# Kernel optimization log

Hardware: AMD Instinct MI355X
Metric: run time of the kernel (lower is better)

The kernel has to match this reference:

```python
import jax, jax.numpy as jnp
import numpy as np

B, N, E = 4, 10000, 160000
IN, OUT, H, ED = 64, 128, 2, 1
SLOPE = 0.2  # GATv2Conv default negative_slope


def _seg_softmax(logits, seg, n):
    # logits: [Ef, H]; softmax over edges sharing the same dst node, per head
    m = jax.ops.segment_max(logits, seg, num_segments=n)
    e = jnp.exp(logits - m[seg])
    d = jax.ops.segment_sum(e, seg, num_segments=n)
    return e / d[seg]


def setup_inputs() -> dict:
    key = jax.random.key(0)
    ks = jax.random.split(key, 10)
    s = 0.05
    return {
        "node_feats": jax.random.normal(ks[0], (B, N, IN), jnp.float32),
        "edge_index": jax.random.randint(ks[1], (2, E), 0, N, dtype=jnp.int64),
        "edge_attr": jax.random.normal(ks[2], (E, ED), jnp.float32),
        "Wl": jax.random.normal(ks[3], (IN, H * OUT), jnp.float32) * s,
        "bl": jax.random.normal(ks[4], (H * OUT,), jnp.float32) * s,
        "Wr": jax.random.normal(ks[5], (IN, H * OUT), jnp.float32) * s,
        "br": jax.random.normal(ks[6], (H * OUT,), jnp.float32) * s,
        "We": jax.random.normal(ks[7], (ED, H * OUT), jnp.float32) * s,
        "att": jax.random.normal(ks[8], (H, OUT), jnp.float32) * s,
        "bias": jax.random.normal(ks[9], (H * OUT,), jnp.float32) * s,
    }


def reference(node_feats, edge_index, edge_attr, Wl, bl, Wr, br, We, att, bias):
    src, dst = edge_index[0], edge_index[1]
    # PyG add_self_loops(fill_value='mean'): self-loop attr = mean of incoming edge attrs per node
    ones = jnp.ones((E,), edge_attr.dtype)
    deg = jax.ops.segment_sum(ones, dst, num_segments=N)
    loop_attr = jax.ops.segment_sum(edge_attr, dst, num_segments=N) / jnp.maximum(deg, 1.0)[:, None]
    sl = jnp.arange(N)
    src_f = jnp.concatenate([src, sl])           # [Ef] with Ef = E + N
    dst_f = jnp.concatenate([dst, sl])
    e_feat = (jnp.concatenate([edge_attr, loop_attr], axis=0) @ We).reshape(-1, H, OUT)  # [Ef,H,C]

    xl = (node_feats @ Wl + bl).reshape(B, N, H, OUT)  # lin_l(x)
    xr = (node_feats @ Wr + br).reshape(B, N, H, OUT)  # lin_r(x)

    # GATv2: score on leaky_relu(x_l[src] + x_r[dst] + lin_edge(e))
    msg = jax.nn.leaky_relu(xl[:, src_f] + xr[:, dst_f] + e_feat[None], SLOPE)  # [B,Ef,H,C]
    logits = jnp.einsum('behc,hc->beh', msg, att)                               # [B,Ef,H]
    alpha = jax.vmap(lambda l: _seg_softmax(l, dst_f, N))(logits)               # [B,Ef,H]

    weighted = alpha[..., None] * xl[:, src_f]                                  # [B,Ef,H,C]
    out = jax.vmap(lambda w: jax.ops.segment_sum(w, dst_f, num_segments=N))(weighted)  # [B,N,H,C]
    return out.reshape(B, N, H * OUT) + bias
```

## Files before the change

### kernel.cpp

```cpp
#include <hip/hip_runtime.h>
#include <hip/hip_bf16.h>

#define BQ 4
#define NN 10000
#define EE 160000
#define HC 256
#define SLOPEK 0.2f
#define CAPE 128

typedef __attribute__((ext_vector_type(8))) short bf16x8;
typedef __attribute__((ext_vector_type(4))) float f32x4;

__device__ __forceinline__ unsigned short f2bf(float f) {
    unsigned int u = __float_as_uint(f);
    u = (u + 0x7FFFu + ((u >> 16) & 1u)) >> 16;
    return (unsigned short)u;
}
__device__ __forceinline__ float bflo(unsigned int u) { return __uint_as_float(u << 16); }
__device__ __forceinline__ float bfhi(unsigned int u) { return __uint_as_float(u & 0xFFFF0000u); }

__global__ __launch_bounds__(256) void k_wpack(
    const float* __restrict__ Wl, const float* __restrict__ bl,
    const float* __restrict__ Wr, const float* __restrict__ br,
    unsigned short* __restrict__ wp, float* __restrict__ bp)
{
    const int tid = blockIdx.x * 256 + threadIdx.x;
    if (tid < 32768) {
        const int j  = tid & 7;
        const int l  = (tid >> 3) & 63;
        const int s  = (tid >> 9) & 1;
        const int ct = tid >> 10;
        const int col = ct * 16 + (l & 15);
        const int kk  = s * 32 + ((l >> 4) << 3) + j;
        const float w = (col < 256) ? Wl[kk * 256 + col] : Wr[kk * 256 + (col - 256)];
        wp[tid] = f2bf(w);
    } else if (tid < 32768 + 512) {
        const int c = tid - 32768;
        bp[c] = (c < 256) ? bl[c] : br[c - 256];
    }
}

__global__ __launch_bounds__(256) void k_pre(
    const float* __restrict__ x, const unsigned short* __restrict__ wp,
    const float* __restrict__ bp,
    unsigned short* __restrict__ xl, unsigned short* __restrict__ xr,
    const int* __restrict__ ei, const float* __restrict__ ea,
    int* __restrict__ cnt, float* __restrict__ asum,
    int* __restrict__ csrc, float* __restrict__ cattr)
{
    if (blockIdx.x >= 625) {
        const int e = (blockIdx.x - 625) * 256 + threadIdx.x;
        const int   sn = ei[e];
        const int   d  = ei[EE + e];
        const float a  = ea[e];
        const int pos  = atomicAdd(&cnt[d], 1);
        atomicAdd(&asum[d], a);
        if (pos < CAPE - 1) {
            csrc[d * CAPE + pos]  = sn << 10;
            cattr[d * CAPE + pos] = a;
        }
        return;
    }
    const int w = threadIdx.x >> 6, l = threadIdx.x & 63;
    const int row0 = blockIdx.x * 64 + w * 16;
    const int arow = row0 + (l & 15);
    const float* xp = x + (size_t)arow * 64 + ((l >> 4) << 3);

    bf16x8 a[2];
#pragma unroll
    for (int s = 0; s < 2; ++s) {
        const float4 lo = *reinterpret_cast<const float4*>(xp + s * 32);
        const float4 hi = *reinterpret_cast<const float4*>(xp + s * 32 + 4);
        union { bf16x8 v; unsigned short u[8]; } t;
        t.u[0] = f2bf(lo.x); t.u[1] = f2bf(lo.y); t.u[2] = f2bf(lo.z); t.u[3] = f2bf(lo.w);
        t.u[4] = f2bf(hi.x); t.u[5] = f2bf(hi.y); t.u[6] = f2bf(hi.z); t.u[7] = f2bf(hi.w);
        a[s] = t.v;
    }
    const int colb = l & 15;
    const int rsub = (l >> 4) << 2;

    for (int g = 0; g < 8; ++g) {
        f32x4 acc[4] = {{0.f,0.f,0.f,0.f},{0.f,0.f,0.f,0.f},
                        {0.f,0.f,0.f,0.f},{0.f,0.f,0.f,0.f}};
#pragma unroll
        for (int c = 0; c < 4; ++c) {
            const int ct = g * 4 + c;
            const bf16x8 b0 = *reinterpret_cast<const bf16x8*>(wp + (((ct * 2 + 0) * 64 + l) << 3));
            const bf16x8 b1 = *reinterpret_cast<const bf16x8*>(wp + (((ct * 2 + 1) * 64 + l) << 3));
            acc[c] = __builtin_amdgcn_mfma_f32_16x16x32_bf16(a[0], b0, acc[c], 0, 0, 0);
            acc[c] = __builtin_amdgcn_mfma_f32_16x16x32_bf16(a[1], b1, acc[c], 0, 0, 0);
        }
#pragma unroll
        for (int c = 0; c < 4; ++c) {
            const int col = (g * 4 + c) * 16 + colb;
            const float bv = bp[col];
#pragma unroll
            for (int r = 0; r < 4; ++r) {
                const int row = row0 + rsub + r;
                const int bb = (row >= 20000) ? (row >= 30000 ? 3 : 2)
                                              : (row >= 10000 ? 1 : 0);
                const int n = row - bb * NN;
                const unsigned short h = f2bf(acc[c][r] + bv);
                if (col < 256) xl[(((size_t)(n * 4 + bb)) << 8) + col] = h;
                else           xr[(((size_t)(n * 4 + bb)) << 8) + (col - 256)] = h;
            }
        }
    }
}

__global__ __launch_bounds__(256, 4) void k_gat(
    const unsigned short* __restrict__ xl, const unsigned short* __restrict__ xr,
    const int* __restrict__ cnt, const float* __restrict__ asum,
    const int* __restrict__ csrc, const float* __restrict__ cattr,
    const float* __restrict__ We, const float* __restrict__ att,
    const float* __restrict__ bias, float* __restrict__ outp)
{
    const int t  = threadIdx.x;
    const int wv = t >> 6, ln = t & 63;
    const int n  = blockIdx.x * 4 + wv;
    const int c  = ln & 15;
    const int b  = ln >> 4;
    const int ch0 = c << 4;

    int dg = cnt[n];
    if (dg > 63) dg = 63;
    int   ms = csrc[n * CAPE + ln];
    float ma = cattr[n * CAPE + ln];
    if (ln == dg) {
        ms = n << 10;
        ma = asum[n] / fmaxf((float)dg, 1.0f);
    }
    const int ntot = dg + 1;

    float we16[16], at16[16], xr16[16], acc[16];
    {
        const float4* Wp = reinterpret_cast<const float4*>(We + ch0);
        const float4* Ap = reinterpret_cast<const float4*>(att + ch0);
#pragma unroll
        for (int j = 0; j < 4; ++j) {
            const float4 w4 = Wp[j], a4 = Ap[j];
            we16[4*j+0] = w4.x; we16[4*j+1] = w4.y; we16[4*j+2] = w4.z; we16[4*j+3] = w4.w;
            at16[4*j+0] = a4.x; at16[4*j+1] = a4.y; at16[4*j+2] = a4.z; at16[4*j+3] = a4.w;
        }
        const uint4* Xp = reinterpret_cast<const uint4*>(
            xr + ((size_t)n << 10) + (b << 8) + ch0);
        const uint4 r0 = Xp[0], r1 = Xp[1];
        xr16[0]=bflo(r0.x); xr16[1]=bfhi(r0.x); xr16[2]=bflo(r0.y); xr16[3]=bfhi(r0.y);
        xr16[4]=bflo(r0.z); xr16[5]=bfhi(r0.z); xr16[6]=bflo(r0.w); xr16[7]=bfhi(r0.w);
        xr16[8]=bflo(r1.x); xr16[9]=bfhi(r1.x); xr16[10]=bflo(r1.y); xr16[11]=bfhi(r1.y);
        xr16[12]=bflo(r1.z); xr16[13]=bfhi(r1.z); xr16[14]=bflo(r1.w); xr16[15]=bfhi(r1.w);
    }
#pragma unroll
    for (int k = 0; k < 16; ++k) acc[k] = 0.f;
    float sh = 0.f;

    const unsigned short* __restrict__ xlp = xl + (b << 8) + ch0;

    int   s0 = __builtin_amdgcn_readlane(ms, 0);
    float a0 = __int_as_float(__builtin_amdgcn_readlane(__float_as_int(ma), 0));
    const unsigned short* pp = xlp + s0;
    uint4 A  = *reinterpret_cast<const uint4*>(pp);
    uint4 Bv = *reinterpret_cast<const uint4*>(pp + 8);

    for (int i = 0; i < ntot; ++i) {
        const int ip = (i + 1 < ntot) ? i + 1 : i;
        const int   s1 = __builtin_amdgcn_readlane(ms, ip);
        const float a1 = __int_as_float(__builtin_amdgcn_readlane(__float_as_int(ma), ip));
        const unsigned short* pn = xlp + s1;
        const uint4 A2 = *reinterpret_cast<const uint4*>(pn);
        const uint4 B2 = *reinterpret_cast<const uint4*>(pn + 8);

        float xv[16];
        xv[0]=bflo(A.x);  xv[1]=bfhi(A.x);  xv[2]=bflo(A.y);  xv[3]=bfhi(A.y);
        xv[4]=bflo(A.z);  xv[5]=bfhi(A.z);  xv[6]=bflo(A.w);  xv[7]=bfhi(A.w);
        xv[8]=bflo(Bv.x); xv[9]=bfhi(Bv.x); xv[10]=bflo(Bv.y); xv[11]=bfhi(Bv.y);
        xv[12]=bflo(Bv.z); xv[13]=bfhi(Bv.z); xv[14]=bflo(Bv.w); xv[15]=bfhi(Bv.w);

        float q[4];
#pragma unroll
        for (int g = 0; g < 4; ++g) {
            float v = fmaf(a0, we16[4*g], xv[4*g] + xr16[4*g]);
            v = fmaf(SLOPEK - 1.f, fminf(v, 0.f), v);
            float qq = v * at16[4*g];
#pragma unroll
            for (int k = 1; k < 4; ++k) {
                float u = fmaf(a0, we16[4*g+k], xv[4*g+k] + xr16[4*g+k]);
                u = fmaf(SLOPEK - 1.f, fminf(u, 0.f), u);
                qq = fmaf(u, at16[4*g+k], qq);
            }
            q[g] = qq;
        }
        float p = (q[0] + q[1]) + (q[2] + q[3]);
        p += __shfl_xor(p, 1);
        p += __shfl_xor(p, 2);
        p += __shfl_xor(p, 4);
        const float e = __expf(p);
        sh += e;
#pragma unroll
        for (int k = 0; k < 16; ++k) acc[k] = fmaf(e, xv[k], acc[k]);

        A = A2; Bv = B2; a0 = a1;
    }

    const float inv = 1.0f / sh;
    float* ob = outp + (((size_t)(b * NN + n)) << 8) + ch0;
    const float4* Bp = reinterpret_cast<const float4*>(bias + ch0);
#pragma unroll
    for (int j = 0; j < 4; ++j) {
        const float4 b4 = Bp[j];
        float4 o;
        o.x = fmaf(acc[4*j+0], inv, b4.x);
        o.y = fmaf(acc[4*j+1], inv, b4.y);
        o.z = fmaf(acc[4*j+2], inv, b4.z);
        o.w = fmaf(acc[4*j+3], inv, b4.w);
        reinterpret_cast<float4*>(ob)[j] = o;
    }
}

extern "C" void kernel_launch(void* const* d_in, const int* in_sizes, int n_in,
                              void* d_out, int out_size, void* d_ws, size_t ws_size,
                              hipStream_t stream)
{
    (void)in_sizes; (void)n_in; (void)out_size; (void)ws_size;
    const float* x    = (const float*)d_in[0];
    const int*   ei   = (const int*)d_in[1];
    const float* ea   = (const float*)d_in[2];
    const float* Wl   = (const float*)d_in[3];
    const float* bl   = (const float*)d_in[4];
    const float* Wr   = (const float*)d_in[5];
    const float* br   = (const float*)d_in[6];
    const float* We   = (const float*)d_in[7];
    const float* att  = (const float*)d_in[8];
    const float* bias = (const float*)d_in[9];
    float* outp = (float*)d_out;

    const size_t R = (size_t)BQ * NN;
    unsigned short* xl16 = (unsigned short*)d_ws;
    unsigned short* xr16 = xl16 + R * HC;
    int*   cnt   = (int*)(xr16 + R * HC);
    float* asum  = (float*)(cnt + NN);
    int*   csrc  = (int*)(asum + NN);
    float* cattr = (float*)(csrc + (size_t)NN * CAPE);
    unsigned short* wp = (unsigned short*)(cattr + (size_t)NN * CAPE);
    float* bp    = (float*)(wp + 32768);

    hipMemsetAsync(cnt, 0, sizeof(int) * NN * 2, stream);

    k_wpack<<<130, 256, 0, stream>>>(Wl, bl, Wr, br, wp, bp);
    k_pre  <<<1250, 256, 0, stream>>>(x, wp, bp, xl16, xr16,
                                      ei, ea, cnt, asum, csrc, cattr);
    k_gat  <<<NN / 4, 256, 0, stream>>>(xl16, xr16, cnt, asum, csrc, cattr,
                                        We, att, bias, outp);
}
```

Baseline: 99.56 us.

## Split each node's edge loop across four wavefronts and pack edge metadata

The GAT kernel now assigns one destination node per block, and its four wavefronts each process every fourth incoming edge. Partial softmax numerators and denominators are then combined through shared memory before the output is written. Edge source offset and attribute are packed into a single int2 array, so each edge needs one store and one load instead of two. The split shortens the serial per-node edge chain and quadruples the grid, at the cost of a block barrier, shared-memory traffic, and four times the redundant setup loads of xr, We and att per node.

```diff
diff --git a/kernel.cpp b/kernel.cpp
--- a/kernel.cpp
+++ b/kernel.cpp
@@ -46,7 +46,7 @@
     unsigned short* __restrict__ xl, unsigned short* __restrict__ xr,
     const int* __restrict__ ei, const float* __restrict__ ea,
     int* __restrict__ cnt, float* __restrict__ asum,
-    int* __restrict__ csrc, float* __restrict__ cattr)
+    int2* __restrict__ cmeta)
 {
     if (blockIdx.x >= 625) {
         const int e = (blockIdx.x - 625) * 256 + threadIdx.x;
@@ -55,10 +55,8 @@
         const float a  = ea[e];
         const int pos  = atomicAdd(&cnt[d], 1);
         atomicAdd(&asum[d], a);
-        if (pos < CAPE - 1) {
-            csrc[d * CAPE + pos]  = sn << 10;
-            cattr[d * CAPE + pos] = a;
-        }
+        if (pos < CAPE - 1)
+            cmeta[d * CAPE + pos] = make_int2(sn << 10, __float_as_int(a));
         return;
     }
     const int w = threadIdx.x >> 6, l = threadIdx.x & 63;
@@ -111,21 +109,25 @@
 __global__ __launch_bounds__(256, 4) void k_gat(
     const unsigned short* __restrict__ xl, const unsigned short* __restrict__ xr,
     const int* __restrict__ cnt, const float* __restrict__ asum,
-    const int* __restrict__ csrc, const float* __restrict__ cattr,
+    const int2* __restrict__ cmeta,
     const float* __restrict__ We, const float* __restrict__ att,
     const float* __restrict__ bias, float* __restrict__ outp)
 {
     const int t  = threadIdx.x;
     const int wv = t >> 6, ln = t & 63;
-    const int n  = blockIdx.x * 4 + wv;
+    const int n  = blockIdx.x;
     const int c  = ln & 15;
     const int b  = ln >> 4;
     const int ch0 = c << 4;
 
+    __shared__ float sAcc[4][64][20];
+    __shared__ float sSh[4][64];
+
     int dg = cnt[n];
     if (dg > 63) dg = 63;
-    int   ms = csrc[n * CAPE + ln];
-    float ma = cattr[n * CAPE + ln];
+    const int2 md0 = cmeta[n * CAPE + ln];
+    int   ms = md0.x;
+    float ma = __int_as_float(md0.y);
     if (ln == dg) {
         ms = n << 10;
         ma = asum[n] / fmaxf((float)dg, 1.0f);
@@ -156,14 +158,17 @@
 
     const unsigned short* __restrict__ xlp = xl + (b << 8) + ch0;
 
-    int   s0 = __builtin_amdgcn_readlane(ms, 0);
-    float a0 = __int_as_float(__builtin_amdgcn_readlane(__float_as_int(ma), 0));
-    const unsigned short* pp = xlp + s0;
-    uint4 A  = *reinterpret_cast<const uint4*>(pp);
-    uint4 Bv = *reinterpret_cast<const uint4*>(pp + 8);
-
-    for (int i = 0; i < ntot; ++i) {
-        const int ip = (i + 1 < ntot) ? i + 1 : i;
+    uint4 A, Bv;
+    float a0 = 0.f;
+    if (wv < ntot) {
+        const int   s0 = __builtin_amdgcn_readlane(ms, wv);
+        a0 = __int_as_float(__builtin_amdgcn_readlane(__float_as_int(ma), wv));
+        const unsigned short* pp = xlp + s0;
+        A  = *reinterpret_cast<const uint4*>(pp);
+        Bv = *reinterpret_cast<const uint4*>(pp + 8);
+    }
+    for (int i = wv; i < ntot; i += 4) {
+        const int ip = (i + 4 < ntot) ? i + 4 : i;
         const int   s1 = __builtin_amdgcn_readlane(ms, ip);
         const float a1 = __int_as_float(__builtin_amdgcn_readlane(__float_as_int(ma), ip));
         const unsigned short* pn = xlp + s1;
@@ -202,19 +207,30 @@
         A = A2; Bv = B2; a0 = a1;
     }
 
-    const float inv = 1.0f / sh;
-    float* ob = outp + (((size_t)(b * NN + n)) << 8) + ch0;
-    const float4* Bp = reinterpret_cast<const float4*>(bias + ch0);
 #pragma unroll
     for (int j = 0; j < 4; ++j) {
-        const float4 b4 = Bp[j];
-        float4 o;
-        o.x = fmaf(acc[4*j+0], inv, b4.x);
-        o.y = fmaf(acc[4*j+1], inv, b4.y);
-        o.z = fmaf(acc[4*j+2], inv, b4.z);
-        o.w = fmaf(acc[4*j+3], inv, b4.w);
-        reinterpret_cast<float4*>(ob)[j] = o;
-    }
+        const float4 v = make_float4(acc[4*j+0], acc[4*j+1], acc[4*j+2], acc[4*j+3]);
+        *reinterpret_cast<float4*>(&sAcc[wv][ln][4*j]) = v;
+    }
+    sSh[wv][ln] = sh;
+    __syncthreads();
+
+    float4 s = make_float4(0.f, 0.f, 0.f, 0.f);
+    float shT = 0.f;
+#pragma unroll
+    for (int w = 0; w < 4; ++w) {
+        const float4 a4 = *reinterpret_cast<const float4*>(&sAcc[w][ln][4*wv]);
+        s.x += a4.x; s.y += a4.y; s.z += a4.z; s.w += a4.w;
+        shT += sSh[w][ln];
+    }
+    const float inv = 1.0f / shT;
+    const float4 b4 = reinterpret_cast<const float4*>(bias + ch0)[wv];
+    float4 o;
+    o.x = fmaf(s.x, inv, b4.x);
+    o.y = fmaf(s.y, inv, b4.y);
+    o.z = fmaf(s.z, inv, b4.z);
+    o.w = fmaf(s.w, inv, b4.w);
+    reinterpret_cast<float4*>(outp + (((size_t)(b * NN + n)) << 8) + ch0)[wv] = o;
 }
 
 extern "C" void kernel_launch(void* const* d_in, const int* in_sizes, int n_in,
@@ -239,16 +255,15 @@
     unsigned short* xr16 = xl16 + R * HC;
     int*   cnt   = (int*)(xr16 + R * HC);
     float* asum  = (float*)(cnt + NN);
-    int*   csrc  = (int*)(asum + NN);
-    float* cattr = (float*)(csrc + (size_t)NN * CAPE);
-    unsigned short* wp = (unsigned short*)(cattr + (size_t)NN * CAPE);
+    int2*  cmeta = (int2*)(asum + NN);
+    unsigned short* wp = (unsigned short*)(cmeta + (size_t)NN * CAPE);
     float* bp    = (float*)(wp + 32768);
 
     hipMemsetAsync(cnt, 0, sizeof(int) * NN * 2, stream);
 
     k_wpack<<<130, 256, 0, stream>>>(Wl, bl, Wr, br, wp, bp);
     k_pre  <<<1250, 256, 0, stream>>>(x, wp, bp, xl16, xr16,
-                                      ei, ea, cnt, asum, csrc, cattr);
-    k_gat  <<<NN / 4, 256, 0, stream>>>(xl16, xr16, cnt, asum, csrc, cattr,
-                                        We, att, bias, outp);
-}
+                                      ei, ea, cnt, asum, cmeta);
+    k_gat  <<<NN, 256, 0, stream>>>(xl16, xr16, cnt, asum, cmeta,
+                                    We, att, bias, outp);
+}
```

Result: slower. 103.2 us (+3.6%).

## Deepen gather prefetch to four slots and pack edge metadata as int2

Applied to the files above, without the earlier changes.

The per-node aggregation loop now keeps four rotating register slots of prefetched source features instead of one, so several gathers are in flight while earlier edges are computed. Edge source index and attribute are stored together in one int2 array, so a single load fetches both. The degree is made wave-uniform with readfirstlane, and the occupancy hint on launch bounds is removed. More in-flight loads raise register pressure and may lower occupancy.

```diff
diff --git a/kernel.cpp b/kernel.cpp
--- a/kernel.cpp
+++ b/kernel.cpp
@@ -46,7 +46,7 @@
     unsigned short* __restrict__ xl, unsigned short* __restrict__ xr,
     const int* __restrict__ ei, const float* __restrict__ ea,
     int* __restrict__ cnt, float* __restrict__ asum,
-    int* __restrict__ csrc, float* __restrict__ cattr)
+    int2* __restrict__ cmeta)
 {
     if (blockIdx.x >= 625) {
         const int e = (blockIdx.x - 625) * 256 + threadIdx.x;
@@ -55,10 +55,8 @@
         const float a  = ea[e];
         const int pos  = atomicAdd(&cnt[d], 1);
         atomicAdd(&asum[d], a);
-        if (pos < CAPE - 1) {
-            csrc[d * CAPE + pos]  = sn << 10;
-            cattr[d * CAPE + pos] = a;
-        }
+        if (pos < CAPE - 1)
+            cmeta[d * CAPE + pos] = make_int2(sn << 10, __float_as_int(a));
         return;
     }
     const int w = threadIdx.x >> 6, l = threadIdx.x & 63;
@@ -108,10 +106,10 @@
     }
 }
 
-__global__ __launch_bounds__(256, 4) void k_gat(
+__global__ __launch_bounds__(256) void k_gat(
     const unsigned short* __restrict__ xl, const unsigned short* __restrict__ xr,
     const int* __restrict__ cnt, const float* __restrict__ asum,
-    const int* __restrict__ csrc, const float* __restrict__ cattr,
+    const int2* __restrict__ cmeta,
     const float* __restrict__ We, const float* __restrict__ att,
     const float* __restrict__ bias, float* __restrict__ outp)
 {
@@ -122,10 +120,12 @@
     const int b  = ln >> 4;
     const int ch0 = c << 4;
 
-    int dg = cnt[n];
-    if (dg > 63) dg = 63;
-    int   ms = csrc[n * CAPE + ln];
-    float ma = cattr[n * CAPE + ln];
+    int dg0 = cnt[n];
+    if (dg0 > 63) dg0 = 63;
+    const int dg = __builtin_amdgcn_readfirstlane(dg0);
+    const int2 md0 = cmeta[n * CAPE + ln];
+    int   ms = md0.x;
+    float ma = __int_as_float(md0.y);
     if (ln == dg) {
         ms = n << 10;
         ma = asum[n] / fmaxf((float)dg, 1.0f);
@@ -156,20 +156,20 @@
 
     const unsigned short* __restrict__ xlp = xl + (b << 8) + ch0;
 
-    int   s0 = __builtin_amdgcn_readlane(ms, 0);
-    float a0 = __int_as_float(__builtin_amdgcn_readlane(__float_as_int(ma), 0));
-    const unsigned short* pp = xlp + s0;
-    uint4 A  = *reinterpret_cast<const uint4*>(pp);
-    uint4 Bv = *reinterpret_cast<const uint4*>(pp + 8);
-
-    for (int i = 0; i < ntot; ++i) {
-        const int ip = (i + 1 < ntot) ? i + 1 : i;
-        const int   s1 = __builtin_amdgcn_readlane(ms, ip);
-        const float a1 = __int_as_float(__builtin_amdgcn_readlane(__float_as_int(ma), ip));
-        const unsigned short* pn = xlp + s1;
-        const uint4 A2 = *reinterpret_cast<const uint4*>(pn);
-        const uint4 B2 = *reinterpret_cast<const uint4*>(pn + 8);
-
+    uint4 A0, B0, A1, B1, A2, B2, A3, B3;
+    float ea0, ea1, ea2, ea3;
+
+#define LOADSLOT(S, IDX) do { \
+        const int ii_ = (IDX); \
+        const int ic_ = ii_ < dg ? ii_ : dg; \
+        const int   s_ = __builtin_amdgcn_readlane(ms, ic_); \
+        ea##S = __int_as_float(__builtin_amdgcn_readlane(__float_as_int(ma), ic_)); \
+        const unsigned short* p_ = xlp + s_; \
+        A##S = *reinterpret_cast<const uint4*>(p_); \
+        B##S = *reinterpret_cast<const uint4*>(p_ + 8); \
+    } while (0)
+
+    auto edgeC = [&](const uint4& A, const uint4& Bv, float a0) {
         float xv[16];
         xv[0]=bflo(A.x);  xv[1]=bfhi(A.x);  xv[2]=bflo(A.y);  xv[3]=bfhi(A.y);
         xv[4]=bflo(A.z);  xv[5]=bfhi(A.z);  xv[6]=bflo(A.w);  xv[7]=bfhi(A.w);
@@ -198,9 +198,23 @@
         sh += e;
 #pragma unroll
         for (int k = 0; k < 16; ++k) acc[k] = fmaf(e, xv[k], acc[k]);
-
-        A = A2; Bv = B2; a0 = a1;
-    }
+    };
+
+    LOADSLOT(0, 0);
+    LOADSLOT(1, 1);
+    LOADSLOT(2, 2);
+
+    int i = 0;
+    for (; i + 3 < ntot; i += 4) {
+        LOADSLOT(3, i + 3); edgeC(A0, B0, ea0);
+        LOADSLOT(0, i + 4); edgeC(A1, B1, ea1);
+        LOADSLOT(1, i + 5); edgeC(A2, B2, ea2);
+        LOADSLOT(2, i + 6); edgeC(A3, B3, ea3);
+    }
+    if (i     < ntot) edgeC(A0, B0, ea0);
+    if (i + 1 < ntot) edgeC(A1, B1, ea1);
+    if (i + 2 < ntot) edgeC(A2, B2, ea2);
+#undef LOADSLOT
 
     const float inv = 1.0f / sh;
     float* ob = outp + (((size_t)(b * NN + n)) << 8) + ch0;
@@ -239,16 +253,15 @@
     unsigned short* xr16 = xl16 + R * HC;
     int*   cnt   = (int*)(xr16 + R * HC);
     float* asum  = (float*)(cnt + NN);
-    int*   csrc  = (int*)(asum + NN);
-    float* cattr = (float*)(csrc + (size_t)NN * CAPE);
-    unsigned short* wp = (unsigned short*)(cattr + (size_t)NN * CAPE);
+    int2*  cmeta = (int2*)(asum + NN);
+    unsigned short* wp = (unsigned short*)(cmeta + (size_t)NN * CAPE);
     float* bp    = (float*)(wp + 32768);
 
     hipMemsetAsync(cnt, 0, sizeof(int) * NN * 2, stream);
 
     k_wpack<<<130, 256, 0, stream>>>(Wl, bl, Wr, br, wp, bp);
     k_pre  <<<1250, 256, 0, stream>>>(x, wp, bp, xl16, xr16,
-                                      ei, ea, cnt, asum, csrc, cattr);
-    k_gat  <<<NN / 4, 256, 0, stream>>>(xl16, xr16, cnt, asum, csrc, cattr,
+                                      ei, ea, cnt, asum, cmeta);
+    k_gat  <<<NN / 4, 256, 0, stream>>>(xl16, xr16, cnt, asum, cmeta,
                                         We, att, bias, outp);
 }
```

Result: faster. 95.81 us (-3.8%).
